# Optimization experiments

Measured on AMD Instinct MI355X. Metric: run time of the kernel, lower is better.

Reference implementation:

```python
import jax, jax.numpy as jnp
import numpy as np
from jax import lax

BATCH, SEQ, IN_DIM, STATE, OUT_DIM = 8, 4096, 256, 256, 256


def setup_inputs() -> dict:
    key = jax.random.key(0)
    kx, ka, kb, kc = jax.random.split(key, 4)
    x = jax.random.normal(kx, (BATCH, SEQ, IN_DIM), dtype=jnp.float32)
    # A initialized as randn normalized by its largest singular value (spectral norm)
    A_init = jax.random.normal(ka, (STATE, STATE), dtype=jnp.float32)
    s_max = jnp.linalg.svd(A_init, compute_uv=False)[0]
    A = A_init / (s_max + 1e-8)
    B = jax.random.normal(kb, (IN_DIM, STATE), dtype=jnp.float32) / IN_DIM
    C = jax.random.normal(kc, (STATE, OUT_DIM), dtype=jnp.float32) / STATE
    h0 = jnp.zeros((STATE,), dtype=jnp.float32)
    return {"x": x, "A": A, "B": B, "C": C, "h0": h0}


def reference(x, A, B, C, h0):
    # h_{t} = h_{t-1} @ A + x_t @ B ;  y_t = h_t @ C
    bsz = x.shape[0]
    xB = jnp.einsum('bsi,in->sbn', x, B)  # precompute input projections, time-major
    h_init = jnp.broadcast_to(h0, (bsz, h0.shape[0]))

    def step(h, xb_t):
        h = h @ A + xb_t
        return h, h

    _, hs = lax.scan(step, h_init, xB)  # hs: [S, B, N]
    y = jnp.einsum('sbn,no->bso', hs, C)  # [B, S, O]
    return y
```

## Files before the change

kernel.cpp:

```cpp
#include <hip/hip_runtime.h>


#define SEQ    4096
#define NBATCH 8
#define ND     256
#define CHUNK  8
#define NCHUNK 512
#define LOSC   2048.0f
#define LOINV  (1.0f/2048.0f)

typedef _Float16 fp16_t;
typedef __attribute__((ext_vector_type(8))) _Float16 f16x8;
typedef __attribute__((ext_vector_type(4))) _Float16 f16x4;
typedef __attribute__((ext_vector_type(4))) float f32x4;

__global__ __launch_bounds__(64) void prep_frags3(
    const float* __restrict__ A, const float* __restrict__ B,
    const float* __restrict__ C,
    fp16_t* __restrict__ fAh, fp16_t* __restrict__ fAl,
    fp16_t* __restrict__ fBh, fp16_t* __restrict__ fBl,
    fp16_t* __restrict__ fCh, fp16_t* __restrict__ fCl) {
  const int which = blockIdx.x >> 7;
  const int blk   = blockIdx.x & 127;
  const float* M = (which == 0) ? A : (which == 1) ? B : C;
  fp16_t* hi = (which == 0) ? fAh : (which == 1) ? fBh : fCh;
  fp16_t* lo = (which == 0) ? fAl : (which == 1) ? fBl : fCl;
  const int lane = threadIdx.x;
  const int tile = blk >> 3, slice = blk & 7;
  const int n  = tile * 16 + (lane & 15);
  const int k0 = slice * 32 + (lane >> 4) * 8;
  f16x8 vh, vl;
  #pragma unroll
  for (int j = 0; j < 8; ++j) {
    const float v = M[(size_t)(k0 + j) * ND + n];
    const fp16_t h = (fp16_t)v;
    vh[j] = h;
    vl[j] = (fp16_t)((v - (float)h) * LOSC);
  }
  const size_t fo = ((size_t)blk * 64 + lane) * 8;
  *(f16x8*)&hi[fo] = vh;
  *(f16x8*)&lo[fo] = vl;
}

__global__ __launch_bounds__(1024, 2) void mfma_gemm(const float* __restrict__ X,
                                                     const fp16_t* __restrict__ Mhi,
                                                     const fp16_t* __restrict__ Mlo,
                                                     float* __restrict__ Out,
                                                     int mode) {
  const int m0   = blockIdx.x * 64;
  const int tid  = threadIdx.x;
  const int lane = tid & 63;
  const int w    = tid >> 6;
  const int br   = lane & 15;
  const int akg  = lane >> 4;

  __shared__ fp16_t Xh[32 * 512];
  __shared__ fp16_t Xl[32 * 512];
  char* Xhb = (char*)Xh;
  char* Xlb = (char*)Xl;

  #pragma unroll
  for (int pass = 0; pass < 2; ++pass) {
    const int tau = pass * 1024 + tid;
    const int row = tau >> 5;
    const int sub = tau & 31;
    const int s   = sub >> 2;
    const int ak  = sub & 3;
    const int m = m0 + row;
    const size_t in_row = (mode == 0)
        ? ((size_t)(m & 7) * SEQ + (m >> 3))
        : (size_t)m;
    const float* xp = &X[in_row * ND + s * 32 + ak * 8];
    const float4 x0 = *(const float4*)(xp);
    const float4 x1 = *(const float4*)(xp + 4);
    const float a[8] = {x0.x, x0.y, x0.z, x0.w, x1.x, x1.y, x1.z, x1.w};
    f16x8 vh, vl;
    #pragma unroll
    for (int j = 0; j < 8; ++j) {
      const fp16_t h = (fp16_t)a[j];
      vh[j] = h;
      vl[j] = (fp16_t)((a[j] - (float)h) * LOSC);
    }
    const int off = (((row >> 4) * 8 + s) << 10) +
                    (((ak << 4) | (row & 15)) ^ s) * 16;
    *(f16x8*)(Xhb + off) = vh;
    *(f16x8*)(Xlb + off) = vl;
  }

  f16x8 MH[8], ML[8];
  #pragma unroll
  for (int s = 0; s < 8; ++s) {
    const size_t fo = (((size_t)w * 8 + s) * 64 + lane) * 8;
    MH[s] = *(const f16x8*)&Mhi[fo];
    ML[s] = *(const f16x8*)&Mlo[fo];
  }
  __syncthreads();

  f32x4 accm[4], accl[4];
  #pragma unroll
  for (int mt = 0; mt < 4; ++mt) {
    accm[mt] = (f32x4)0.0f;
    accl[mt] = (f32x4)0.0f;
  }

  #pragma unroll
  for (int s = 0; s < 8; ++s) {
    #pragma unroll
    for (int mt = 0; mt < 4; ++mt) {
      const int byte = ((mt * 8 + s) << 10) + ((((akg << 4) | br) ^ s) << 4);
      const f16x8 bh = *(const f16x8*)(Xhb + byte);
      const f16x8 bl = *(const f16x8*)(Xlb + byte);
      accm[mt] = __builtin_amdgcn_mfma_f32_16x16x32_f16(MH[s], bh, accm[mt], 0, 0, 0);
      accl[mt] = __builtin_amdgcn_mfma_f32_16x16x32_f16(ML[s], bh, accl[mt], 0, 0, 0);
      accl[mt] = __builtin_amdgcn_mfma_f32_16x16x32_f16(MH[s], bl, accl[mt], 0, 0, 0);
    }
  }

  #pragma unroll
  for (int mt = 0; mt < 4; ++mt) {
    const int m = m0 + mt * 16 + br;
    const size_t out_row = (mode == 1)
        ? ((size_t)(m & 7) * SEQ + (m >> 3))
        : (size_t)m;
    float4 o;
    o.x = accm[mt][0] + accl[mt][0] * LOINV;
    o.y = accm[mt][1] + accl[mt][1] * LOINV;
    o.z = accm[mt][2] + accl[mt][2] * LOINV;
    o.w = accm[mt][3] + accl[mt][3] * LOINV;
    *(float4*)&Out[out_row * ND + w * 16 + akg * 4] = o;
  }
}

__global__ __launch_bounds__(1024, 2) void mfma_rscan(
    const fp16_t* __restrict__ Mh, const fp16_t* __restrict__ Ml,
    const float* __restrict__ Init,
    const float* In,
    float* OutEach,
    float* __restrict__ OutFinal,
    int nupd, int gstride, int nseq, int init_bcast, int entry_mode) {
  const int seq0 = blockIdx.x * 2;
  const int tid  = threadIdx.x;
  const int lane = tid & 63;
  const int w    = tid >> 6;
  const int br   = lane & 15;
  const int akg  = lane >> 4;

  __shared__ fp16_t hH[2][8 * 512];
  __shared__ fp16_t hL[2][8 * 512];

  {
    const int task = tid >> 1;
    const int half = tid & 1;
    const int row  = task & 15;
    const int s    = (task >> 4) & 7;
    const int ak   = task >> 7;
    const int sq = seq0 + (row >> 3);
    const int b  = row & 7;
    const int c0 = s * 32 + ak * 8 + half * 4;
    f32x4 v = (f32x4)0.0f;
    if (Init != nullptr && sq < nseq) {
      const size_t off = init_bcast ? (size_t)c0
                                    : ((size_t)sq * NBATCH + b) * ND + c0;
      v = *(const f32x4*)&Init[off];
      if (entry_mode && OutEach != nullptr)
        *(f32x4*)&OutEach[((size_t)sq * gstride * NBATCH + b) * ND + c0] = v;
    }
    f16x4 vh, vl;
    #pragma unroll
    for (int j = 0; j < 4; ++j) {
      const fp16_t h = (fp16_t)v[j];
      vh[j] = h;
      vl[j] = (fp16_t)((v[j] - (float)h) * LOSC);
    }
    const int off = (s << 10) + ((((ak << 4) | row) ^ s) << 4) + half * 8;
    *(f16x4*)((char*)hH[0] + off) = vh;
    *(f16x4*)((char*)hL[0] + off) = vl;
  }

  f16x8 AH[8], AL[8];
  #pragma unroll
  for (int s = 0; s < 8; ++s) {
    const size_t fo = (((size_t)w * 8 + s) * 64 + lane) * 8;
    AH[s] = *(const f16x8*)&Mh[fo];
    AL[s] = *(const f16x8*)&Ml[fo];
  }
  __syncthreads();

  const int sq   = seq0 + (br >> 3);
  const int b    = br & 7;
  const bool live = (sq < nseq);
  const int sqc  = live ? sq : (nseq - 1);
  const int col0 = w * 16 + akg * 4;

  int rdoff[8];
  #pragma unroll
  for (int s = 0; s < 8; ++s)
    rdoff[s] = (s << 10) + ((((akg << 4) | br) ^ s) << 4);
  const int sw   = col0 >> 5;
  const int akr  = (col0 >> 3) & 3;
  const int wroff = (sw << 10) + ((((akr << 4) | br) ^ sw) << 4) + (col0 & 7) * 2;

  f32x4 uv = *(const f32x4*)&In[((size_t)(sqc * gstride) * NBATCH + b) * ND + col0];
  f32x4 uvn;
  f32x4 res;
  int p = 0;
  for (int j = 0; j < nupd; ++j) {
    if (j + 1 < nupd)
      uvn = *(const f32x4*)&In[((size_t)(sqc * gstride + j + 1) * NBATCH + b) * ND + col0];
    const char* rH = (const char*)hH[p];
    const char* rL = (const char*)hL[p];
    f32x4 accm = uv, acclA = (f32x4)0.0f, acclB = (f32x4)0.0f;
    #pragma unroll
    for (int s = 0; s < 8; ++s) {
      const f16x8 bh = *(const f16x8*)(rH + rdoff[s]);
      const f16x8 bl = *(const f16x8*)(rL + rdoff[s]);
      accm  = __builtin_amdgcn_mfma_f32_16x16x32_f16(AH[s], bh, accm,  0, 0, 0);
      acclA = __builtin_amdgcn_mfma_f32_16x16x32_f16(AL[s], bh, acclA, 0, 0, 0);
      acclB = __builtin_amdgcn_mfma_f32_16x16x32_f16(AH[s], bl, acclB, 0, 0, 0);
    }
    #pragma unroll
    for (int r = 0; r < 4; ++r) res[r] = accm[r] + (acclA[r] + acclB[r]) * LOINV;
    {
      f16x4 vh, vl;
      #pragma unroll
      for (int r = 0; r < 4; ++r) {
        const fp16_t hh = (fp16_t)res[r];
        vh[r] = hh;
        vl[r] = (fp16_t)((res[r] - (float)hh) * LOSC);
      }
      *(f16x4*)((char*)hH[p ^ 1] + wroff) = vh;
      *(f16x4*)((char*)hL[p ^ 1] + wroff) = vl;
    }
    if (OutEach != nullptr && live) {
      const size_t pos = entry_mode ? (size_t)(sq * gstride + j + 1)
                                    : (size_t)(sq * gstride + j);
      *(f32x4*)&OutEach[(pos * NBATCH + b) * ND + col0] = res;
    }
    uv = uvn;
    p ^= 1;
    __syncthreads();
  }

  if (OutFinal != nullptr && live)
    *(f32x4*)&OutFinal[((size_t)sq * NBATCH + b) * ND + col0] = res;
}

__global__ __launch_bounds__(256) void gemm256(const float* __restrict__ X,
                                               const float* __restrict__ Y,
                                               float* __restrict__ Out) {
  const int m0 = blockIdx.x * 4;
  const int n  = threadIdx.x;
  __shared__ float Xs[ND][4];
  #pragma unroll
  for (int r = 0; r < 4; ++r) Xs[n][r] = X[(m0 + r) * ND + n];
  __syncthreads();
  float a0 = 0.f, a1 = 0.f, a2 = 0.f, a3 = 0.f;
  #pragma unroll 8
  for (int k = 0; k < ND; ++k) {
    const float yv = Y[k * ND + n];
    const float4 xv = *(const float4*)&Xs[k][0];
    a0 = fmaf(xv.x, yv, a0);
    a1 = fmaf(xv.y, yv, a1);
    a2 = fmaf(xv.z, yv, a2);
    a3 = fmaf(xv.w, yv, a3);
  }
  Out[(m0 + 0) * ND + n] = a0;
  Out[(m0 + 1) * ND + n] = a1;
  Out[(m0 + 2) * ND + n] = a2;
  Out[(m0 + 3) * ND + n] = a3;
}

extern "C" void kernel_launch(void* const* d_in, const int* in_sizes, int n_in,
                              void* d_out, int out_size, void* d_ws, size_t ws_size,
                              hipStream_t stream) {
  const float* x  = (const float*)d_in[0];
  const float* A  = (const float*)d_in[1];
  const float* Bm = (const float*)d_in[2];
  const float* Cm = (const float*)d_in[3];
  const float* h0 = (const float*)d_in[4];
  float* y = (float*)d_out;

  float* U     = (float*)d_ws;
  float* t0    = U + (size_t)SEQ * NBATCH * ND;
  float* t1    = t0 + ND * ND;
  float* A8f   = t1 + ND * ND;
  float* A64f  = A8f + ND * ND;
  float* A512f = A64f + ND * ND;
  float* E     = A512f + ND * ND;
  float* S1    = E + (size_t)NCHUNK * NBATCH * ND;
  float* S2    = S1 + (size_t)64 * NBATCH * ND;
  float* G3    = S2 + (size_t)8 * NBATCH * ND;
  float* Hc2   = G3 + (size_t)8 * NBATCH * ND;
  float* Hc    = Hc2 + (size_t)64 * NBATCH * ND;
  fp16_t* fA_hi   = (fp16_t*)(Hc + (size_t)NCHUNK * NBATCH * ND);
  fp16_t* fA_lo   = fA_hi + ND * ND;
  fp16_t* fB_hi   = fA_lo + ND * ND;
  fp16_t* fB_lo   = fB_hi + ND * ND;
  fp16_t* fC_hi   = fB_lo + ND * ND;
  fp16_t* fC_lo   = fC_hi + ND * ND;
  fp16_t* fA8_hi  = fC_lo + ND * ND;
  fp16_t* fA8_lo  = fA8_hi + ND * ND;
  fp16_t* fA64_hi = fA8_lo + ND * ND;
  fp16_t* fA64_lo = fA64_hi + ND * ND;
  fp16_t* fA512_hi = fA64_lo + ND * ND;
  fp16_t* fA512_lo = fA512_hi + ND * ND;

  prep_frags3<<<384, 64, 0, stream>>>(A, Bm, Cm, fA_hi, fA_lo, fB_hi, fB_lo,
                                      fC_hi, fC_lo);

  gemm256<<<64, 256, 0, stream>>>(A,    A,    t0);
  gemm256<<<64, 256, 0, stream>>>(t0,   t0,   t1);
  gemm256<<<64, 256, 0, stream>>>(t1,   t1,   A8f);
  gemm256<<<64, 256, 0, stream>>>(A8f,  A8f,  t0);
  gemm256<<<64, 256, 0, stream>>>(t0,   t0,   t1);
  gemm256<<<64, 256, 0, stream>>>(t1,   t1,   A64f);
  gemm256<<<64, 256, 0, stream>>>(A64f, A64f, t0);
  gemm256<<<64, 256, 0, stream>>>(t0,   t0,   t1);
  gemm256<<<64, 256, 0, stream>>>(t1,   t1,   A512f);

  prep_frags3<<<384, 64, 0, stream>>>(A8f, A64f, A512f,
                                      fA8_hi, fA8_lo, fA64_hi, fA64_lo,
                                      fA512_hi, fA512_lo);

  mfma_gemm<<<512, 1024, 0, stream>>>(x, fB_hi, fB_lo, U, 0);

  mfma_rscan<<<NCHUNK / 2, 1024, 0, stream>>>(fA_hi, fA_lo, nullptr, U,
                                              nullptr, E, 8, 8, NCHUNK, 0, 0);

  mfma_rscan<<<32, 1024, 0, stream>>>(fA8_hi, fA8_lo, nullptr, E,
                                      nullptr, S1, 8, 8, 64, 0, 0);

  mfma_rscan<<<4, 1024, 0, stream>>>(fA64_hi, fA64_lo, nullptr, S1,
                                     nullptr, S2, 8, 8, 8, 0, 0);

  mfma_rscan<<<1, 1024, 0, stream>>>(fA512_hi, fA512_lo, h0, S2,
                                     G3, nullptr, 7, 8, 1, 1, 1);

  mfma_rscan<<<4, 1024, 0, stream>>>(fA64_hi, fA64_lo, G3, S1,
                                     Hc2, nullptr, 7, 8, 8, 0, 1);

  mfma_rscan<<<32, 1024, 0, stream>>>(fA8_hi, fA8_lo, Hc2, E,
                                      Hc, nullptr, 7, 8, 64, 0, 1);

  mfma_rscan<<<NCHUNK / 2, 1024, 0, stream>>>(fA_hi, fA_lo, Hc, U,
                                              U, nullptr, 8, 8, NCHUNK, 0, 0);

  mfma_gemm<<<512, 1024, 0, stream>>>(U, fC_hi, fC_lo, y, 1);
}
```

Before: 237.6 us.

## Stage A-high fragments in LDS and single-buffer the scan state

```diff
diff --git a/kernel.cpp b/kernel.cpp
--- a/kernel.cpp
+++ b/kernel.cpp
@@ -131,7 +131,7 @@
   }
 }
 
-__global__ __launch_bounds__(1024, 2) void mfma_rscan(
+__global__ __launch_bounds__(1024, 1) void mfma_rscan(
     const fp16_t* __restrict__ Mh, const fp16_t* __restrict__ Ml,
     const float* __restrict__ Init,
     const float* In,
@@ -145,8 +145,17 @@
   const int br   = lane & 15;
   const int akg  = lane >> 4;
 
-  __shared__ fp16_t hH[2][8 * 512];
-  __shared__ fp16_t hL[2][8 * 512];
+  __shared__ __align__(16) fp16_t fragH[16 * 8 * 64 * 8];
+  __shared__ fp16_t hH[8 * 512];
+  __shared__ fp16_t hL[8 * 512];
+
+  {
+    const f16x8* src = (const f16x8*)Mh;
+    f16x8* dst = (f16x8*)fragH;
+    #pragma unroll
+    for (int i = 0; i < 8; ++i)
+      dst[i * 1024 + tid] = src[i * 1024 + tid];
+  }
 
   {
     const int task = tid >> 1;
@@ -173,16 +182,8 @@
       vl[j] = (fp16_t)((v[j] - (float)h) * LOSC);
     }
     const int off = (s << 10) + ((((ak << 4) | row) ^ s) << 4) + half * 8;
-    *(f16x4*)((char*)hH[0] + off) = vh;
-    *(f16x4*)((char*)hL[0] + off) = vl;
-  }
-
-  f16x8 AH[8], AL[8];
-  #pragma unroll
-  for (int s = 0; s < 8; ++s) {
-    const size_t fo = (((size_t)w * 8 + s) * 64 + lane) * 8;
-    AH[s] = *(const f16x8*)&Mh[fo];
-    AL[s] = *(const f16x8*)&Ml[fo];
+    *(f16x4*)((char*)hH + off) = vh;
+    *(f16x4*)((char*)hL + off) = vl;
   }
   __syncthreads();
 
@@ -193,33 +194,40 @@
   const int col0 = w * 16 + akg * 4;
 
   int rdoff[8];
-  #pragma unroll
-  for (int s = 0; s < 8; ++s)
+  int foff[8];
+  #pragma unroll
+  for (int s = 0; s < 8; ++s) {
     rdoff[s] = (s << 10) + ((((akg << 4) | br) ^ s) << 4);
+    foff[s]  = (((w * 8 + s) * 64 + lane) << 4);
+  }
   const int sw   = col0 >> 5;
   const int akr  = (col0 >> 3) & 3;
   const int wroff = (sw << 10) + ((((akr << 4) | br) ^ sw) << 4) + (col0 & 7) * 2;
 
+  const char* fHb = (const char*)fragH;
+  const char* rH  = (const char*)hH;
+  const char* rL  = (const char*)hL;
+
   f32x4 uv = *(const f32x4*)&In[((size_t)(sqc * gstride) * NBATCH + b) * ND + col0];
   f32x4 uvn;
   f32x4 res;
-  int p = 0;
   for (int j = 0; j < nupd; ++j) {
     if (j + 1 < nupd)
       uvn = *(const f32x4*)&In[((size_t)(sqc * gstride + j + 1) * NBATCH + b) * ND + col0];
-    const char* rH = (const char*)hH[p];
-    const char* rL = (const char*)hL[p];
     f32x4 accm = uv, acclA = (f32x4)0.0f, acclB = (f32x4)0.0f;
     #pragma unroll
     for (int s = 0; s < 8; ++s) {
+      const f16x8 AHs = *(const f16x8*)(fHb + foff[s]);
+      const f16x8 ALs = *(const f16x8*)&Ml[(size_t)(foff[s] >> 1)];
       const f16x8 bh = *(const f16x8*)(rH + rdoff[s]);
       const f16x8 bl = *(const f16x8*)(rL + rdoff[s]);
-      accm  = __builtin_amdgcn_mfma_f32_16x16x32_f16(AH[s], bh, accm,  0, 0, 0);
-      acclA = __builtin_amdgcn_mfma_f32_16x16x32_f16(AL[s], bh, acclA, 0, 0, 0);
-      acclB = __builtin_amdgcn_mfma_f32_16x16x32_f16(AH[s], bl, acclB, 0, 0, 0);
+      accm  = __builtin_amdgcn_mfma_f32_16x16x32_f16(AHs, bh, accm,  0, 0, 0);
+      acclA = __builtin_amdgcn_mfma_f32_16x16x32_f16(ALs, bh, acclA, 0, 0, 0);
+      acclB = __builtin_amdgcn_mfma_f32_16x16x32_f16(AHs, bl, acclB, 0, 0, 0);
     }
     #pragma unroll
     for (int r = 0; r < 4; ++r) res[r] = accm[r] + (acclA[r] + acclB[r]) * LOINV;
+    __syncthreads();
     {
       f16x4 vh, vl;
       #pragma unroll
@@ -228,8 +236,8 @@
         vh[r] = hh;
         vl[r] = (fp16_t)((res[r] - (float)hh) * LOSC);
       }
-      *(f16x4*)((char*)hH[p ^ 1] + wroff) = vh;
-      *(f16x4*)((char*)hL[p ^ 1] + wroff) = vl;
+      *(f16x4*)((char*)hH + wroff) = vh;
+      *(f16x4*)((char*)hL + wroff) = vl;
     }
     if (OutEach != nullptr && live) {
       const size_t pos = entry_mode ? (size_t)(sq * gstride + j + 1)
@@ -237,7 +245,6 @@
       *(f32x4*)&OutEach[(pos * NBATCH + b) * ND + col0] = res;
     }
     uv = uvn;
-    p ^= 1;
     __syncthreads();
   }
 
```

Measured after the change: 245.0 us. +3.1%, slower.

## Fuse power chain and spine scans into persistent kernels with grid barriers

Applied to the files above, without the earlier changes.

```diff
diff --git a/kernel.cpp b/kernel.cpp
--- a/kernel.cpp
+++ b/kernel.cpp
@@ -13,6 +13,36 @@
 typedef __attribute__((ext_vector_type(8))) _Float16 f16x8;
 typedef __attribute__((ext_vector_type(4))) _Float16 f16x4;
 typedef __attribute__((ext_vector_type(4))) float f32x4;
+
+__device__ __forceinline__ void gsync(unsigned* c, unsigned target) {
+  __syncthreads();
+  if (threadIdx.x == 0) {
+    __threadfence();
+    atomicAdd(c, 1u);
+    while (__hip_atomic_load(c, __ATOMIC_ACQUIRE, __HIP_MEMORY_SCOPE_AGENT) < target)
+      __builtin_amdgcn_s_sleep(8);
+    __threadfence();
+  }
+  __syncthreads();
+}
+
+__device__ __forceinline__ void prep_unit(const float* M, fp16_t* hi, fp16_t* lo,
+                                          int blk, int lane) {
+  const int tile = blk >> 3, slice = blk & 7;
+  const int n  = tile * 16 + (lane & 15);
+  const int k0 = slice * 32 + (lane >> 4) * 8;
+  f16x8 vh, vl;
+  #pragma unroll
+  for (int j = 0; j < 8; ++j) {
+    const float v = M[(size_t)(k0 + j) * ND + n];
+    const fp16_t h = (fp16_t)v;
+    vh[j] = h;
+    vl[j] = (fp16_t)((v - (float)h) * LOSC);
+  }
+  const size_t fo = ((size_t)blk * 64 + lane) * 8;
+  *(f16x8*)&hi[fo] = vh;
+  *(f16x8*)&lo[fo] = vl;
+}
 
 __global__ __launch_bounds__(64) void prep_frags3(
     const float* __restrict__ A, const float* __restrict__ B,
@@ -25,21 +55,59 @@
   const float* M = (which == 0) ? A : (which == 1) ? B : C;
   fp16_t* hi = (which == 0) ? fAh : (which == 1) ? fBh : fCh;
   fp16_t* lo = (which == 0) ? fAl : (which == 1) ? fBl : fCl;
-  const int lane = threadIdx.x;
-  const int tile = blk >> 3, slice = blk & 7;
-  const int n  = tile * 16 + (lane & 15);
-  const int k0 = slice * 32 + (lane >> 4) * 8;
-  f16x8 vh, vl;
-  #pragma unroll
-  for (int j = 0; j < 8; ++j) {
-    const float v = M[(size_t)(k0 + j) * ND + n];
-    const fp16_t h = (fp16_t)v;
-    vh[j] = h;
-    vl[j] = (fp16_t)((v - (float)h) * LOSC);
-  }
-  const size_t fo = ((size_t)blk * 64 + lane) * 8;
-  *(f16x8*)&hi[fo] = vh;
-  *(f16x8*)&lo[fo] = vl;
+  prep_unit(M, hi, lo, blk, threadIdx.x);
+}
+
+__device__ __forceinline__ void gemm_body(const float* X, const float* Y,
+                                          float* Out, float (*Xs)[4]) {
+  const int m0 = blockIdx.x * 4;
+  const int n  = threadIdx.x;
+  #pragma unroll
+  for (int r = 0; r < 4; ++r) Xs[n][r] = X[(m0 + r) * ND + n];
+  __syncthreads();
+  float a0 = 0.f, a1 = 0.f, a2 = 0.f, a3 = 0.f;
+  #pragma unroll 8
+  for (int k = 0; k < ND; ++k) {
+    const float yv = Y[k * ND + n];
+    const float4 xv = *(const float4*)&Xs[k][0];
+    a0 = fmaf(xv.x, yv, a0);
+    a1 = fmaf(xv.y, yv, a1);
+    a2 = fmaf(xv.z, yv, a2);
+    a3 = fmaf(xv.w, yv, a3);
+  }
+  Out[(m0 + 0) * ND + n] = a0;
+  Out[(m0 + 1) * ND + n] = a1;
+  Out[(m0 + 2) * ND + n] = a2;
+  Out[(m0 + 3) * ND + n] = a3;
+}
+
+__global__ __launch_bounds__(256) void power_chain(
+    const float* __restrict__ A,
+    float* q1, float* q2, float* q3, float* q4, float* q5, float* q6,
+    float* A8f, float* A64f, float* A512f,
+    fp16_t* fA8h, fp16_t* fA8l, fp16_t* fA64h, fp16_t* fA64l,
+    fp16_t* fA512h, fp16_t* fA512l,
+    unsigned* sync) {
+  __shared__ float Xs[ND][4];
+  gemm_body(A,    A,    q1,    Xs);  gsync(sync + 0, 64);
+  gemm_body(q1,   q1,   q2,    Xs);  gsync(sync + 1, 64);
+  gemm_body(q2,   q2,   A8f,   Xs);  gsync(sync + 2, 64);
+  gemm_body(A8f,  A8f,  q3,    Xs);  gsync(sync + 3, 64);
+  gemm_body(q3,   q3,   q4,    Xs);  gsync(sync + 4, 64);
+  gemm_body(q4,   q4,   A64f,  Xs);  gsync(sync + 5, 64);
+  gemm_body(A64f, A64f, q5,    Xs);  gsync(sync + 6, 64);
+  gemm_body(q5,   q5,   q6,    Xs);  gsync(sync + 7, 64);
+  gemm_body(q6,   q6,   A512f, Xs);  gsync(sync + 8, 64);
+  const int gw   = blockIdx.x * 4 + (threadIdx.x >> 6);
+  const int lane = threadIdx.x & 63;
+  for (int u = gw; u < 384; u += 256) {
+    const int which = u >> 7;
+    const int blk   = u & 127;
+    const float* M = (which == 0) ? A8f : (which == 1) ? A64f : A512f;
+    fp16_t* hi = (which == 0) ? fA8h : (which == 1) ? fA64h : fA512h;
+    fp16_t* lo = (which == 0) ? fA8l : (which == 1) ? fA64l : fA512l;
+    prep_unit(M, hi, lo, blk, lane);
+  }
 }
 
 __global__ __launch_bounds__(1024, 2) void mfma_gemm(const float* __restrict__ X,
@@ -131,22 +199,17 @@
   }
 }
 
-__global__ __launch_bounds__(1024, 2) void mfma_rscan(
-    const fp16_t* __restrict__ Mh, const fp16_t* __restrict__ Ml,
-    const float* __restrict__ Init,
-    const float* In,
-    float* OutEach,
-    float* __restrict__ OutFinal,
-    int nupd, int gstride, int nseq, int init_bcast, int entry_mode) {
+__device__ __forceinline__ void rscan_body(
+    const fp16_t* Mh, const fp16_t* Ml,
+    const float* Init, const float* In, float* OutEach, float* OutFinal,
+    int nupd, int gstride, int nseq, int init_bcast, int entry_mode,
+    fp16_t (*hH)[8 * 512], fp16_t (*hL)[8 * 512]) {
   const int seq0 = blockIdx.x * 2;
   const int tid  = threadIdx.x;
   const int lane = tid & 63;
   const int w    = tid >> 6;
   const int br   = lane & 15;
   const int akg  = lane >> 4;
-
-  __shared__ fp16_t hH[2][8 * 512];
-  __shared__ fp16_t hL[2][8 * 512];
 
   {
     const int task = tid >> 1;
@@ -245,29 +308,37 @@
     *(f32x4*)&OutFinal[((size_t)sq * NBATCH + b) * ND + col0] = res;
 }
 
-__global__ __launch_bounds__(256) void gemm256(const float* __restrict__ X,
-                                               const float* __restrict__ Y,
-                                               float* __restrict__ Out) {
-  const int m0 = blockIdx.x * 4;
-  const int n  = threadIdx.x;
-  __shared__ float Xs[ND][4];
-  #pragma unroll
-  for (int r = 0; r < 4; ++r) Xs[n][r] = X[(m0 + r) * ND + n];
-  __syncthreads();
-  float a0 = 0.f, a1 = 0.f, a2 = 0.f, a3 = 0.f;
-  #pragma unroll 8
-  for (int k = 0; k < ND; ++k) {
-    const float yv = Y[k * ND + n];
-    const float4 xv = *(const float4*)&Xs[k][0];
-    a0 = fmaf(xv.x, yv, a0);
-    a1 = fmaf(xv.y, yv, a1);
-    a2 = fmaf(xv.z, yv, a2);
-    a3 = fmaf(xv.w, yv, a3);
-  }
-  Out[(m0 + 0) * ND + n] = a0;
-  Out[(m0 + 1) * ND + n] = a1;
-  Out[(m0 + 2) * ND + n] = a2;
-  Out[(m0 + 3) * ND + n] = a3;
+__global__ __launch_bounds__(1024, 2) void mfma_rscan(
+    const fp16_t* __restrict__ Mh, const fp16_t* __restrict__ Ml,
+    const float* __restrict__ Init,
+    const float* In,
+    float* OutEach,
+    float* __restrict__ OutFinal,
+    int nupd, int gstride, int nseq, int init_bcast, int entry_mode) {
+  __shared__ fp16_t hH[2][8 * 512];
+  __shared__ fp16_t hL[2][8 * 512];
+  rscan_body(Mh, Ml, Init, In, OutEach, OutFinal,
+             nupd, gstride, nseq, init_bcast, entry_mode, hH, hL);
+}
+
+__global__ __launch_bounds__(1024, 2) void spine_scan(
+    const fp16_t* __restrict__ fA8h, const fp16_t* __restrict__ fA8l,
+    const fp16_t* __restrict__ fA64h, const fp16_t* __restrict__ fA64l,
+    const fp16_t* __restrict__ fA512h, const fp16_t* __restrict__ fA512l,
+    const float* __restrict__ h0, const float* __restrict__ E,
+    float* S1, float* S2, float* G3, float* Hc2, float* Hc,
+    unsigned* sync) {
+  __shared__ fp16_t hH[2][8 * 512];
+  __shared__ fp16_t hL[2][8 * 512];
+  rscan_body(fA8h, fA8l, nullptr, E, nullptr, S1, 8, 8, 64, 0, 0, hH, hL);
+  gsync(sync + 16, 32);
+  rscan_body(fA64h, fA64l, nullptr, S1, nullptr, S2, 8, 8, 8, 0, 0, hH, hL);
+  gsync(sync + 17, 32);
+  rscan_body(fA512h, fA512l, h0, S2, G3, nullptr, 7, 8, 1, 1, 1, hH, hL);
+  gsync(sync + 18, 32);
+  rscan_body(fA64h, fA64l, G3, S1, Hc2, nullptr, 7, 8, 8, 0, 1, hH, hL);
+  gsync(sync + 19, 32);
+  rscan_body(fA8h, fA8l, Hc2, E, Hc, nullptr, 7, 8, 64, 0, 1, hH, hL);
 }
 
 extern "C" void kernel_launch(void* const* d_in, const int* in_sizes, int n_in,
@@ -281,9 +352,13 @@
   float* y = (float*)d_out;
 
   float* U     = (float*)d_ws;
-  float* t0    = U + (size_t)SEQ * NBATCH * ND;
-  float* t1    = t0 + ND * ND;
-  float* A8f   = t1 + ND * ND;
+  float* q1    = U + (size_t)SEQ * NBATCH * ND;
+  float* q2    = q1 + ND * ND;
+  float* q3    = q2 + ND * ND;
+  float* q4    = q3 + ND * ND;
+  float* q5    = q4 + ND * ND;
+  float* q6    = q5 + ND * ND;
+  float* A8f   = q6 + ND * ND;
   float* A64f  = A8f + ND * ND;
   float* A512f = A64f + ND * ND;
   float* E     = A512f + ND * ND;
@@ -304,43 +379,26 @@
   fp16_t* fA64_lo = fA64_hi + ND * ND;
   fp16_t* fA512_hi = fA64_lo + ND * ND;
   fp16_t* fA512_lo = fA512_hi + ND * ND;
+  unsigned* sync = (unsigned*)(fA512_lo + ND * ND);
+
+  hipMemsetAsync(sync, 0, 32 * sizeof(unsigned), stream);
 
   prep_frags3<<<384, 64, 0, stream>>>(A, Bm, Cm, fA_hi, fA_lo, fB_hi, fB_lo,
                                       fC_hi, fC_lo);
 
-  gemm256<<<64, 256, 0, stream>>>(A,    A,    t0);
-  gemm256<<<64, 256, 0, stream>>>(t0,   t0,   t1);
-  gemm256<<<64, 256, 0, stream>>>(t1,   t1,   A8f);
-  gemm256<<<64, 256, 0, stream>>>(A8f,  A8f,  t0);
-  gemm256<<<64, 256, 0, stream>>>(t0,   t0,   t1);
-  gemm256<<<64, 256, 0, stream>>>(t1,   t1,   A64f);
-  gemm256<<<64, 256, 0, stream>>>(A64f, A64f, t0);
-  gemm256<<<64, 256, 0, stream>>>(t0,   t0,   t1);
-  gemm256<<<64, 256, 0, stream>>>(t1,   t1,   A512f);
-
-  prep_frags3<<<384, 64, 0, stream>>>(A8f, A64f, A512f,
+  power_chain<<<64, 256, 0, stream>>>(A, q1, q2, q3, q4, q5, q6,
+                                      A8f, A64f, A512f,
                                       fA8_hi, fA8_lo, fA64_hi, fA64_lo,
-                                      fA512_hi, fA512_lo);
+                                      fA512_hi, fA512_lo, sync);
 
   mfma_gemm<<<512, 1024, 0, stream>>>(x, fB_hi, fB_lo, U, 0);
 
   mfma_rscan<<<NCHUNK / 2, 1024, 0, stream>>>(fA_hi, fA_lo, nullptr, U,
                                               nullptr, E, 8, 8, NCHUNK, 0, 0);
 
-  mfma_rscan<<<32, 1024, 0, stream>>>(fA8_hi, fA8_lo, nullptr, E,
-                                      nullptr, S1, 8, 8, 64, 0, 0);
-
-  mfma_rscan<<<4, 1024, 0, stream>>>(fA64_hi, fA64_lo, nullptr, S1,
-                                     nullptr, S2, 8, 8, 8, 0, 0);
-
-  mfma_rscan<<<1, 1024, 0, stream>>>(fA512_hi, fA512_lo, h0, S2,
-                                     G3, nullptr, 7, 8, 1, 1, 1);
-
-  mfma_rscan<<<4, 1024, 0, stream>>>(fA64_hi, fA64_lo, G3, S1,
-                                     Hc2, nullptr, 7, 8, 8, 0, 1);
-
-  mfma_rscan<<<32, 1024, 0, stream>>>(fA8_hi, fA8_lo, Hc2, E,
-                                      Hc, nullptr, 7, 8, 64, 0, 1);
+  spine_scan<<<32, 1024, 0, stream>>>(fA8_hi, fA8_lo, fA64_hi, fA64_lo,
+                                      fA512_hi, fA512_lo, h0, E,
+                                      S1, S2, G3, Hc2, Hc, sync);
 
   mfma_rscan<<<NCHUNK / 2, 1024, 0, stream>>>(fA_hi, fA_lo, Hc, U,
                                               U, nullptr, 8, 8, NCHUNK, 0, 0);
```

Result: slower. 278.7 us (+17.3%).
